# Kernel tuning notes

Measured on AMD Instinct MI355X. Metric: run time of the kernel, lower is better.

## Reference

```python
import math
import jax, jax.numpy as jnp
import numpy as np

N_HEADS = 16

def _alibi_slopes(n_heads: int) -> np.ndarray:
    def pow2_slopes(n):
        start = 2 ** (-2 ** (-(math.log2(n) - 3)))
        return [start * start ** i for i in range(n)]
    if math.log2(n_heads).is_integer():
        slopes = pow2_slopes(n_heads)
    else:
        closest = 2 ** math.floor(math.log2(n_heads))
        slopes = pow2_slopes(closest)
        extra = pow2_slopes(2 * closest)[0::2]
        slopes = slopes + extra[: n_heads - closest]
    return np.asarray(slopes, dtype=np.float32)

def _build_alibi_bias(n_heads: int, T: int) -> jnp.ndarray:
    # (1, H, T, T): lower triangle = -slope*|i-j|, strict upper = -inf (causal)
    slopes = jnp.asarray(_alibi_slopes(n_heads))  # (H,)
    pos = jnp.arange(T)
    dist = pos[None, :] - pos[None, :].T  # (T, T), j - i
    causal = dist < 0  # future positions (j > i means dist>0? note: dist = j - i transposed)
    # match torch: distances = positions[None,:] - positions[:,None] -> dist[i,j] = j - i
    dist = pos[None, :] - pos[:, None]
    causal = dist > 0  # wait: torch masks distances < 0 where distances[i,j] = j - i? No:
    # torch: distances = positions.unsqueeze(0) - positions.unsqueeze(1) -> dist[i,j] = positions[j] - positions[i]? 
    # unsqueeze(0): (1,T) row j; unsqueeze(1): (T,1) row i -> dist[i,j] = pos[j] - pos[i]
    # causal_mask = dist < 0 masks j < i ... but then bias upper triangle kept?
    # Actually torch masks where distances < 0, i.e., j < i (past). That seems inverted,
    # but we must be FAITHFUL: mask fills -inf where pos[j] - pos[i] < 0.
    d = pos[None, :] - pos[:, None]  # d[i,j] = j - i
    mask = d < 0
    bias = -slopes[:, None, None] * jnp.abs(d).astype(jnp.float32)[None, :, :]
    bias = jnp.where(mask[None, :, :], -jnp.inf, bias)
    return bias[None]  # (1, H, T, T)

def setup_inputs() -> dict:
    key = jax.random.key(0)
    k1, k2, k3 = jax.random.split(key, 3)
    B, T, D = 2, 2048, 1024
    x = jax.random.normal(k1, (B, T, D), dtype=jnp.float32)
    W_qkv = jax.random.normal(k2, (D, 3 * D), dtype=jnp.float32) * (1.0 / math.sqrt(D))
    W_out = jax.random.normal(k3, (D, D), dtype=jnp.float32) * (1.0 / math.sqrt(D))
    return {"x": x, "W_qkv": W_qkv, "W_out": W_out}

def reference(x, W_qkv, W_out):
    B, T, D = x.shape
    H = N_HEADS
    hd = D // H
    qkv = x @ W_qkv  # (B, T, 3D)
    q, k, v = jnp.split(qkv, 3, axis=-1)
    q = q.reshape(B, T, H, hd).transpose(0, 2, 1, 3)  # (B,H,T,hd)
    k = k.reshape(B, T, H, hd).transpose(0, 2, 1, 3)
    v = v.reshape(B, T, H, hd).transpose(0, 2, 1, 3)
    scale = 1.0 / math.sqrt(hd)
    attn = jnp.einsum('bhqd,bhkd->bhqk', q, k) * scale  # (B,H,T,T)
    attn = attn + _build_alibi_bias(H, T)
    attn = jax.nn.softmax(attn, axis=-1)
    out = jnp.einsum('bhqk,bhkd->bhqd', attn, v)  # (B,H,T,hd)
    out = out.transpose(0, 2, 1, 3).reshape(B, T, D)
    return out @ W_out
```

## Files before the change

kernel.cpp:

```cpp
#include <hip/hip_runtime.h>

#define DEV __device__ __forceinline__

typedef __attribute__((ext_vector_type(4))) float f32x4;
typedef __attribute__((ext_vector_type(16))) float f32x16;
typedef __attribute__((ext_vector_type(8))) short s16x8;

static constexpr int TB  = 2;
static constexpr int TT  = 2048;
static constexpr int TD  = 1024;
static constexpr int TH  = 16;
static constexpr int THD = 64;
static constexpr int TN3 = 3072;
static constexpr int TM  = TB * TT;

#define WS_FLAG   0u
#define WS_XB     1024u
#define WS_WQKVT  (WS_XB + 8388608u)
#define WS_WOUTT  (WS_WQKVT + 6291456u)
#define WS_QKV    (WS_WOUTT + 2097152u)
#define WS_VT     (WS_QKV + 25165824u)
#define WS_CTX    (WS_VT + 8388608u)

DEV unsigned short f2bf(float f) {
  unsigned int u = __builtin_bit_cast(unsigned int, f);
  u += 0x7FFFu + ((u >> 16) & 1u);
  return (unsigned short)(u >> 16);
}
DEV f32x4 mfma16(s16x8 a, s16x8 b, f32x4 c) {
  return __builtin_amdgcn_mfma_f32_16x16x32_bf16(a, b, c, 0, 0, 0);
}
DEV f32x16 mfma32(s16x8 a, s16x8 b, f32x16 c) {
  return __builtin_amdgcn_mfma_f32_32x32x16_bf16(a, b, c, 0, 0, 0);
}
DEV void gload_lds16(const void* g, void* l) {
  __builtin_amdgcn_global_load_lds(
      (const __attribute__((address_space(1))) void*)g,
      (__attribute__((address_space(3))) void*)l, 16, 0, 0);
}
DEV unsigned int cvtpk(float lo, float hi_) {
  unsigned int r;
  asm("v_cvt_pk_bf16_f32 %0, %1, %2" : "=v"(r) : "v"(lo), "v"(hi_));
  return r;
}
DEV void plswap(unsigned int& a, unsigned int& b) {
  asm("v_permlane32_swap_b32 %0, %1" : "+v"(a), "+v"(b));
}

__global__ __launch_bounds__(256) void detect_kernel(const uint4* __restrict__ probe,
                                                     int* __restrict__ flag) {
  __shared__ int cnt;
  if (threadIdx.x == 0) cnt = 0;
  __syncthreads();
  uint4 v = probe[threadIdx.x];
  int local = 0;
  unsigned int w[4] = {v.x, v.y, v.z, v.w};
#pragma unroll
  for (int k = 0; k < 4; ++k) {
    unsigned int e0 = (w[k] >> 7) & 0xFF;
    unsigned int e1 = (w[k] >> 23) & 0xFF;
    if (e0 >= 135) local++;
    if (e1 >= 135) local++;
  }
  atomicAdd(&cnt, local);
  __syncthreads();
  if (threadIdx.x == 0) flag[0] = (cnt < 100) ? 1 : 0;
}

__global__ __launch_bounds__(256) void prep_kernel(const void* __restrict__ x,
                                                   const void* __restrict__ wqkv,
                                                   const void* __restrict__ wout,
                                                   unsigned short* __restrict__ xb,
                                                   unsigned short* __restrict__ wqkvt,
                                                   unsigned short* __restrict__ woutt,
                                                   const int* __restrict__ flag) {
  __shared__ unsigned short tile[64 * 65];
  const int bid = blockIdx.x;
  const bool bf = (flag[0] != 0);
  if (bid < 1024) {
    const void* W; unsigned short* Wt; int N, k0, n0;
    if (bid < 768) { W = wqkv; Wt = wqkvt; N = TN3; k0 = (bid & 15) * 64; n0 = (bid >> 4) * 64; }
    else { int id = bid - 768; W = wout; Wt = woutt; N = TD; k0 = (id & 15) * 64; n0 = (id >> 4) * 64; }
    for (int e = threadIdx.x; e < 4096; e += 256) {
      int kr = e >> 6, nc = e & 63;
      unsigned short v;
      if (bf) v = ((const unsigned short*)W)[(size_t)(k0 + kr) * N + n0 + nc];
      else    v = f2bf(((const float*)W)[(size_t)(k0 + kr) * N + n0 + nc]);
      tile[kr * 65 + nc] = v;
    }
    __syncthreads();
    for (int e = threadIdx.x; e < 4096; e += 256) {
      int nr = e >> 6, kc = e & 63;
      Wt[(size_t)(n0 + nr) * TD + k0 + kc] = tile[kc * 65 + nr];
    }
  } else {
    int i = (bid - 1024) * 256 + threadIdx.x;
    if (i >= (TM * TD) / 8) return;
    if (bf) {
      ((uint4*)xb)[i] = ((const uint4*)x)[i];
    } else {
      const float* s = (const float*)x + (size_t)i * 8;
      unsigned int w0 = (unsigned int)f2bf(s[0]) | ((unsigned int)f2bf(s[1]) << 16);
      unsigned int w1 = (unsigned int)f2bf(s[2]) | ((unsigned int)f2bf(s[3]) << 16);
      unsigned int w2 = (unsigned int)f2bf(s[4]) | ((unsigned int)f2bf(s[5]) << 16);
      unsigned int w3 = (unsigned int)f2bf(s[6]) | ((unsigned int)f2bf(s[7]) << 16);
      uint4 o; o.x = w0; o.y = w1; o.z = w2; o.w = w3;
      ((uint4*)xb)[i] = o;
    }
  }
}

__global__ __launch_bounds__(512, 2) void gemm_8p_kernel(const unsigned short* __restrict__ A,
                                                         const unsigned short* __restrict__ Bt,
                                                         unsigned short* __restrict__ C,
                                                         unsigned short* __restrict__ vtb,
                                                         int Mn, int Nn, int Kn) {
  __shared__ unsigned short lA[2][256 * 64];
  __shared__ unsigned short lB[2][192 * 64];
  const int tid = threadIdx.x;
  const int lane = tid & 63;
  const int wid = tid >> 6;
  const int wm = wid >> 2, wn = wid & 3;
  const int l15 = lane & 15, lg = lane >> 4;

  const int nby = Nn / 192;
  const int nwg = (Mn >> 8) * nby;
  const int cpx = nwg >> 3;
  const int bid = blockIdx.x;
  const int swz = (bid & 7) * cpx + (bid >> 3);
  const int bm = swz / nby, bn = swz % nby;
  const int row0 = bm << 8, col0 = bn * 192;

  const int srow = tid >> 3;
  const int scol = ((tid & 7) ^ (srow & 7)) * 8;
  const unsigned short* aS = A  + (size_t)(row0 + srow) * Kn + scol;
  const unsigned short* bS = Bt + (size_t)(col0 + srow) * Kn + scol;
  const size_t r64 = (size_t)64 * Kn;

#define STGA(dst, koff) do {                                \
    unsigned short* _d = (dst) + tid * 8;                   \
    const unsigned short* _s = aS + (koff);                 \
    gload_lds16(_s,           _d);                          \
    gload_lds16(_s + r64,     _d + 4096);                   \
    gload_lds16(_s + 2 * r64, _d + 8192);                   \
    gload_lds16(_s + 3 * r64, _d + 12288);                  \
  } while (0)
#define STGB(dst, koff) do {                                \
    unsigned short* _d = (dst) + tid * 8;                   \
    const unsigned short* _s = bS + (koff);                 \
    gload_lds16(_s,           _d);                          \
    gload_lds16(_s + r64,     _d + 4096);                   \
    gload_lds16(_s + 2 * r64, _d + 8192);                   \
  } while (0)

  f32x4 acc[8][3];
#pragma unroll
  for (int m = 0; m < 8; ++m)
#pragma unroll
    for (int n = 0; n < 3; ++n) acc[m][n] = (f32x4){0.f, 0.f, 0.f, 0.f};

  const int sa = l15 & 7;
  const int kc0 = (lg ^ sa) * 8;
  const int kc1 = ((4 + lg) ^ sa) * 8;
  const int aRow = (wm * 128 + l15) * 64;
  const int bRow = (wn * 48 + l15) * 64;

  STGA(&lA[0][0], 0);
  STGB(&lB[0][0], 0);
  asm volatile("s_waitcnt vmcnt(0)" ::: "memory");
  __builtin_amdgcn_s_barrier();

  const int nt = Kn >> 6;
  for (int t = 0; t < nt; ++t) {
    const unsigned short* la = &lA[t & 1][0];
    const unsigned short* lb = &lB[t & 1][0];
    unsigned short* na = &lA[(t + 1) & 1][0];
    unsigned short* nb = &lB[(t + 1) & 1][0];
    const int koff = (t + 1) << 6;
    const bool more = (t + 1 < nt);

    s16x8 af[8], bv[3];

#pragma unroll
    for (int m = 0; m < 8; ++m) af[m] = *(const s16x8*)&la[aRow + m * 1024 + kc0];
#pragma unroll
    for (int n = 0; n < 3; ++n) bv[n] = *(const s16x8*)&lb[bRow + n * 1024 + kc0];
    if (more) STGA(na, koff);
    __builtin_amdgcn_s_barrier();
    asm volatile("s_waitcnt lgkmcnt(0)" ::: "memory");
    __builtin_amdgcn_sched_barrier(0);
    __builtin_amdgcn_s_setprio(1);
#pragma unroll
    for (int m = 0; m < 8; ++m)
#pragma unroll
      for (int n = 0; n < 3; ++n)
        acc[m][n] = mfma16(af[m], bv[n], acc[m][n]);
    __builtin_amdgcn_s_setprio(0);
    __builtin_amdgcn_s_barrier();

#pragma unroll
    for (int m = 0; m < 8; ++m) af[m] = *(const s16x8*)&la[aRow + m * 1024 + kc1];
#pragma unroll
    for (int n = 0; n < 3; ++n) bv[n] = *(const s16x8*)&lb[bRow + n * 1024 + kc1];
    if (more) STGB(nb, koff);
    __builtin_amdgcn_s_barrier();
    asm volatile("s_waitcnt lgkmcnt(0)" ::: "memory");
    __builtin_amdgcn_sched_barrier(0);
    __builtin_amdgcn_s_setprio(1);
#pragma unroll
    for (int m = 0; m < 8; ++m)
#pragma unroll
      for (int n = 0; n < 3; ++n)
        acc[m][n] = mfma16(af[m], bv[n], acc[m][n]);
    __builtin_amdgcn_s_setprio(0);
    asm volatile("s_waitcnt vmcnt(0)" ::: "memory");
    __builtin_amdgcn_s_barrier();
  }
#undef STGA
#undef STGB

  unsigned short* cw = C + (size_t)(row0 + wm * 128 + lg * 4) * Nn + col0 + wn * 48 + l15;
#pragma unroll
  for (int m = 0; m < 8; ++m)
#pragma unroll
    for (int n = 0; n < 3; ++n) {
      const int cbase = col0 + wn * 48 + n * 16;
      if (cbase < 2048) {
#pragma unroll
        for (int j = 0; j < 4; ++j)
          cw[(size_t)(m * 16 + j) * Nn + n * 16] = f2bf(acc[m][n][j]);
      } else {
        int tg = row0 + wm * 128 + lg * 4 + m * 16;
        int bb = tg >> 11, tt = tg & 2047;
        int cc2 = cbase + l15 - 2048;
        int h = cc2 >> 6, d = cc2 & 63;
        unsigned short* dst = vtb + (((size_t)(bb * 16 + h) * 64 + d) << 11) + tt;
        uint2 pk;
        pk.x = cvtpk(acc[m][n][0], acc[m][n][1]);
        pk.y = cvtpk(acc[m][n][2], acc[m][n][3]);
        *(uint2*)dst = pk;
      }
    }
}

__global__ __launch_bounds__(256, 2) void gemm_bt2_kernel(const unsigned short* __restrict__ A,
                                                          const unsigned short* __restrict__ Bt,
                                                          void* __restrict__ Cout,
                                                          int Mn, int Nn, int Kn,
                                                          const int* __restrict__ flag) {
  __shared__ unsigned short lA[3][128 * 64];
  __shared__ unsigned short lB[3][64 * 64];
  const int tid  = threadIdx.x;
  const int lane = tid & 63, wid = tid >> 6;
  const int wr = wid >> 1, wc = wid & 1;
  const int l15 = lane & 15, lg = lane >> 4;
  const int row0 = blockIdx.x * 128, col0 = blockIdx.y * 64;

  f32x4 acc[4][2];
#pragma unroll
  for (int m = 0; m < 4; ++m)
#pragma unroll
    for (int n = 0; n < 2; ++n) acc[m][n] = (f32x4){0.f, 0.f, 0.f, 0.f};

  const int srow = tid >> 3;
  const int scol = ((tid & 7) ^ (srow & 7)) * 8;
  const unsigned short* aS = A  + (size_t)(row0 + srow) * Kn + scol;
  const unsigned short* bS = Bt + (size_t)(col0 + srow) * Kn + scol;
  const size_t r32 = (size_t)32 * Kn;

#define STG2(bi, koff) do {                                                 \
    unsigned short* _da = &lA[bi][0] + tid * 8;                             \
    unsigned short* _db = &lB[bi][0] + tid * 8;                             \
    gload_lds16(aS + (koff),            _da);                               \
    gload_lds16(aS + (koff) + r32,      _da + 2048);                        \
    gload_lds16(aS + (koff) + 2 * r32,  _da + 4096);                        \
    gload_lds16(aS + (koff) + 3 * r32,  _da + 6144);                        \
    gload_lds16(bS + (koff),            _db);                               \
    gload_lds16(bS + (koff) + r32,      _db + 2048);                        \
  } while (0)

  const int sa = l15 & 7;
  const int kc0 = (lg ^ sa) * 8;
  const int kc1 = ((4 + lg) ^ sa) * 8;
  const int aoff = (wr * 64 + l15) * 64;
  const int boff = (wc * 32 + l15) * 64;

  const int nt = Kn >> 6;
  STG2(0, 0);
  STG2(1, 64);
  asm volatile("s_waitcnt vmcnt(6)" ::: "memory");
  __builtin_amdgcn_s_barrier();

  int cur = 0;
  for (int t = 0; t < nt; ++t) {
    const unsigned short* la = &lA[cur][0];
    const unsigned short* lb = &lB[cur][0];
    const bool deep = (t + 2 < nt);

    s16x8 af[4], bfv[2];
#pragma unroll
    for (int m = 0; m < 4; ++m) af[m] = *(const s16x8*)&la[aoff + m * 1024 + kc0];
#pragma unroll
    for (int n = 0; n < 2; ++n) bfv[n] = *(const s16x8*)&lb[boff + n * 1024 + kc0];
    if (deep) { int nbuf = (cur + 2 == 3) ? 0 : ((cur + 2 == 4) ? 1 : cur + 2); STG2(nbuf, (t + 2) << 6); }
    __builtin_amdgcn_s_barrier();
    asm volatile("s_waitcnt lgkmcnt(0)" ::: "memory");
    __builtin_amdgcn_sched_barrier(0);
    __builtin_amdgcn_s_setprio(1);
#pragma unroll
    for (int m = 0; m < 4; ++m)
#pragma unroll
      for (int n = 0; n < 2; ++n)
        acc[m][n] = mfma16(af[m], bfv[n], acc[m][n]);
    __builtin_amdgcn_s_setprio(0);
    __builtin_amdgcn_s_barrier();

#pragma unroll
    for (int m = 0; m < 4; ++m) af[m] = *(const s16x8*)&la[aoff + m * 1024 + kc1];
#pragma unroll
    for (int n = 0; n < 2; ++n) bfv[n] = *(const s16x8*)&lb[boff + n * 1024 + kc1];
    __builtin_amdgcn_s_barrier();
    asm volatile("s_waitcnt lgkmcnt(0)" ::: "memory");
    __builtin_amdgcn_sched_barrier(0);
    __builtin_amdgcn_s_setprio(1);
#pragma unroll
    for (int m = 0; m < 4; ++m)
#pragma unroll
      for (int n = 0; n < 2; ++n)
        acc[m][n] = mfma16(af[m], bfv[n], acc[m][n]);
    __builtin_amdgcn_s_setprio(0);
    if (t + 1 < nt) {
      if (deep) asm volatile("s_waitcnt vmcnt(6)" ::: "memory");
      else      asm volatile("s_waitcnt vmcnt(0)" ::: "memory");
      __builtin_amdgcn_s_barrier();
    }
    cur = (cur == 2) ? 0 : cur + 1;
  }
#undef STG2

  const bool obf = (flag[0] != 0);
#pragma unroll
  for (int m = 0; m < 4; ++m)
#pragma unroll
    for (int n = 0; n < 2; ++n)
#pragma unroll
      for (int j = 0; j < 4; ++j) {
        int r = row0 + wr * 64 + m * 16 + lg * 4 + j;
        int c = col0 + wc * 32 + n * 16 + l15;
        if (obf) ((unsigned short*)Cout)[(size_t)r * Nn + c] = f2bf(acc[m][n][j]);
        else     ((float*)Cout)[(size_t)r * Nn + c] = acc[m][n][j];
      }
}

__global__ __launch_bounds__(256, 4) void attn_kernel(const unsigned short* __restrict__ qkv,
                                                      const unsigned short* __restrict__ vt,
                                                      unsigned short* __restrict__ ctx) {
  __shared__ __align__(16) unsigned char smem[32768];
  unsigned short* kl0 = (unsigned short*)smem;
  unsigned short* vl0 = (unsigned short*)(smem + 16384);
  float* red = (float*)smem;

  const int bid = blockIdx.x;
  const int r_ = bid & 255, q_ = bid >> 8;
  const int s_ = r_ >> 5, g_ = r_ & 31;
  const int bh = (g_ + 8 * q_) & 31;
  const int x32 = (q_ == 0) ? s_ : (q_ == 1) ? 15 - s_ : (q_ == 2) ? 16 + s_ : 31 - s_;
  const int b = bh >> 4, h = bh & 15;

  const int tid = threadIdx.x;
  const int wid = tid >> 6, lane = tid & 63;
  const int wr = wid & 1, wk = wid >> 1;
  const int l31 = lane & 31, hi = lane >> 5;
  const int i_base = x32 * 64 + wr * 32;

  const unsigned short* qb  = qkv + (size_t)b * TT * TN3 + h * THD;
  const unsigned short* kb_ = qkv + (size_t)b * TT * TN3 + TD + h * THD;
  const unsigned short* vb_ = vt + (size_t)bh * THD * TT;

  const float LOG2E = 1.44269504f;
  const float SL2 = exp2f(-0.5f * (float)(h + 1)) * LOG2E;
  const float SC2 = 0.125f * LOG2E;
  const float dbias = -SL2 * 64.0f;

  const int t_rel = (int)((140.0f / SL2 + 63.0f) * (1.0f / 64.0f)) + 1;
  const int t_end = (32 < x32 + t_rel) ? 32 : x32 + t_rel;

  const int srow = tid >> 3;
  const int sx = ((tid & 7) ^ (srow & 7)) * 8;
  const unsigned short* srcK = kb_ + (size_t)(x32 * 64 + srow) * TN3 + sx;
  const unsigned short* srcV = vb_ + (size_t)srow * TT + x32 * 64 + sx;
  const size_t kstep = (size_t)64 * TN3;

#define STAGE(bufi) do {                                   \
    unsigned short* _dk = kl0 + (bufi) * 4096 + tid * 8;   \
    unsigned short* _dv = vl0 + (bufi) * 4096 + tid * 8;   \
    gload_lds16(srcK,            _dk);                     \
    gload_lds16(srcK + 32 * TN3, _dk + 2048);              \
    gload_lds16(srcV,            _dv);                     \
    gload_lds16(srcV + 32 * TT,  _dv + 2048);              \
  } while (0)

  s16x8 qa[4];
  {
    const unsigned short* qr = qb + (size_t)(i_base + l31) * TN3 + hi * 8;
#pragma unroll
    for (int dd = 0; dd < 4; ++dd) qa[dd] = *(const s16x8*)(qr + dd * 16);
  }

  s16x8 ones;
  {
    short ov = (l31 == 0) ? (short)0x3F80 : (short)0;
#pragma unroll
    for (int e = 0; e < 8; ++e) ones[e] = ov;
  }

  float base[16];
#pragma unroll
  for (int r = 0; r < 16; ++r) {
    int cr0 = (r & 3) + 8 * (r >> 2);
    base[r] = -SL2 * (float)(wk * 32 + cr0 + 4 * hi - wr * 32 - l31) - 16.0f;
  }

  f32x16 o0, o1, ol;
#pragma unroll
  for (int r = 0; r < 16; ++r) { o0[r] = 0.f; o1[r] = 0.f; ol[r] = 0.f; }

  const int sw = (l31 & 7) << 4;
  int cc[4];
#pragma unroll
  for (int dd = 0; dd < 4; ++dd) cc[dd] = ((dd * 32 + hi * 16) ^ sw) >> 1;

  int cur = 0;
  STAGE(0); srcK += kstep; srcV += 64;
  asm volatile("s_waitcnt vmcnt(0)" ::: "memory");
  __syncthreads();

  for (int t = x32; t < t_end; ++t) {
    if (t + 1 < t_end) { STAGE(cur ^ 1); srcK += kstep; srcV += 64; }

    const unsigned short* kb = kl0 + cur * 4096;
    const unsigned short* vbl = vl0 + cur * 4096;

    f32x16 sv;
#pragma unroll
    for (int r = 0; r < 16; ++r) sv[r] = 0.f;
    __builtin_amdgcn_s_setprio(1);
#pragma unroll
    for (int dd = 0; dd < 4; ++dd) {
      s16x8 k0 = *(const s16x8*)&kb[(wk * 32 + l31) * 64 + cc[dd]];
      sv = mfma32(k0, qa[dd], sv);
    }
    __builtin_amdgcn_s_setprio(0);

    if (t == x32) {
#pragma unroll
      for (int r = 0; r < 16; ++r) {
        float bb = base[r];
        float v = __builtin_amdgcn_exp2f(fmaf(sv[r], SC2, bb));
        sv[r] = (bb > -15.999f) ? 0.0f : v;
      }
    } else {
#pragma unroll
      for (int r = 0; r < 16; ++r)
        sv[r] = __builtin_amdgcn_exp2f(fmaf(sv[r], SC2, base[r]));
    }
#pragma unroll
    for (int r = 0; r < 16; ++r) base[r] += dbias;

    s16x8 pa[2];
#pragma unroll
    for (int mh = 0; mh < 2; ++mh) {
      unsigned int a0 = cvtpk(sv[8 * mh + 0], sv[8 * mh + 1]);
      unsigned int a1 = cvtpk(sv[8 * mh + 2], sv[8 * mh + 3]);
      unsigned int b0 = cvtpk(sv[8 * mh + 4], sv[8 * mh + 5]);
      unsigned int b1 = cvtpk(sv[8 * mh + 6], sv[8 * mh + 7]);
      plswap(a0, b0); plswap(a1, b1);
      uint4 u; u.x = a0; u.y = a1; u.z = b0; u.w = b1;
      pa[mh] = __builtin_bit_cast(s16x8, u);
    }

    __builtin_amdgcn_s_setprio(1);
#pragma unroll
    for (int ks = 0; ks < 2; ++ks) {
      s16x8 v0 = *(const s16x8*)&vbl[l31 * 64 + cc[wk * 2 + ks]];
      s16x8 v1 = *(const s16x8*)&vbl[(32 + l31) * 64 + cc[wk * 2 + ks]];
      o0 = mfma32(pa[ks], v0, o0);
      o1 = mfma32(pa[ks], v1, o1);
      ol = mfma32(pa[ks], ones, ol);
    }
    __builtin_amdgcn_s_setprio(0);

    asm volatile("s_waitcnt vmcnt(0)" ::: "memory");
    __syncthreads();
    cur ^= 1;
  }
#undef STAGE

  const int rbase = (wr * 64 + lane) * 49;
  if (wk == 1) {
#pragma unroll
    for (int r = 0; r < 16; ++r) red[rbase + r] = o0[r];
#pragma unroll
    for (int r = 0; r < 16; ++r) red[rbase + 16 + r] = o1[r];
#pragma unroll
    for (int r = 0; r < 16; ++r) red[rbase + 32 + r] = ol[r];
  }
  __syncthreads();
  if (wk == 0) {
#pragma unroll
    for (int r = 0; r < 16; ++r) o0[r] += red[rbase + r];
#pragma unroll
    for (int r = 0; r < 16; ++r) o1[r] += red[rbase + 16 + r];
#pragma unroll
    for (int r = 0; r < 16; ++r) ol[r] += red[rbase + 32 + r];

    float rdiv[16];
#pragma unroll
    for (int r = 0; r < 16; ++r) rdiv[r] = 1.0f / __shfl(ol[r], lane & 32);

    unsigned short* cb = ctx + (size_t)(b * TT + i_base) * TD + h * THD + l31;
#pragma unroll
    for (int r = 0; r < 16; ++r) {
      int row = (r & 3) + 8 * (r >> 2) + 4 * hi;
      unsigned int pk = cvtpk(o0[r] * rdiv[r], o1[r] * rdiv[r]);
      cb[(size_t)row * TD] = (unsigned short)pk;
      cb[(size_t)row * TD + 32] = (unsigned short)(pk >> 16);
    }
  }
}

extern "C" void kernel_launch(void* const* d_in, const int* in_sizes, int n_in,
                              void* d_out, int out_size, void* d_ws, size_t ws_size,
                              hipStream_t stream) {
  const void* x    = d_in[0];
  const void* wqkv = d_in[1];
  const void* wout = d_in[2];
  char* ws = (char*)d_ws;
  int* flag             = (int*)(ws + WS_FLAG);
  unsigned short* xb    = (unsigned short*)(ws + WS_XB);
  unsigned short* wqkvt = (unsigned short*)(ws + WS_WQKVT);
  unsigned short* woutt = (unsigned short*)(ws + WS_WOUTT);
  unsigned short* qkvb  = (unsigned short*)(ws + WS_QKV);
  unsigned short* vtb   = (unsigned short*)(ws + WS_VT);
  unsigned short* ctxb  = (unsigned short*)(ws + WS_CTX);

  detect_kernel<<<1, 256, 0, stream>>>((const uint4*)x, flag);
  prep_kernel<<<3072, 256, 0, stream>>>(x, wqkv, wout, xb, wqkvt, woutt, flag);
  gemm_8p_kernel<<<(TM / 256) * (TN3 / 192), 512, 0, stream>>>(xb, wqkvt, qkvb, vtb, TM, TN3, TD);
  attn_kernel<<<1024, 256, 0, stream>>>(qkvb, vtb, ctxb);
  gemm_bt2_kernel<<<dim3(TM / 128, TD / 64), 256, 0, stream>>>(ctxb, woutt, d_out, TM, TD, TD, flag);
}
```

Baseline: 103.1 us.

## Skip bf16 input copy and simplify QKV GEMM k-loop to single-barrier schedule

When the input is already bf16, the prep kernel no longer copies x into the workspace, and the QKV GEMM reads x directly through a flag-selected base pointer. The main k-loop now issues both A and B global-to-LDS prefetches at the start of each iteration. It then loads both k-halves of fragments at once and runs all MFMAs in one block, dropping the intermediate barriers and priority hints. This cuts barrier count and a redundant copy, at the cost of more register pressure and less fine-grained interleaving of loads and MFMAs. The prefetch now writes the other LDS buffer while this iteration reads the current one, so safety relies on the trailing barrier.

```diff
diff --git a/kernel.cpp b/kernel.cpp
--- a/kernel.cpp
+++ b/kernel.cpp
@@ -94,27 +94,26 @@
       Wt[(size_t)(n0 + nr) * TD + k0 + kc] = tile[kc * 65 + nr];
     }
   } else {
+    if (bf) return;
     int i = (bid - 1024) * 256 + threadIdx.x;
     if (i >= (TM * TD) / 8) return;
-    if (bf) {
-      ((uint4*)xb)[i] = ((const uint4*)x)[i];
-    } else {
-      const float* s = (const float*)x + (size_t)i * 8;
-      unsigned int w0 = (unsigned int)f2bf(s[0]) | ((unsigned int)f2bf(s[1]) << 16);
-      unsigned int w1 = (unsigned int)f2bf(s[2]) | ((unsigned int)f2bf(s[3]) << 16);
-      unsigned int w2 = (unsigned int)f2bf(s[4]) | ((unsigned int)f2bf(s[5]) << 16);
-      unsigned int w3 = (unsigned int)f2bf(s[6]) | ((unsigned int)f2bf(s[7]) << 16);
-      uint4 o; o.x = w0; o.y = w1; o.z = w2; o.w = w3;
-      ((uint4*)xb)[i] = o;
-    }
-  }
-}
-
-__global__ __launch_bounds__(512, 2) void gemm_8p_kernel(const unsigned short* __restrict__ A,
+    const float* s = (const float*)x + (size_t)i * 8;
+    unsigned int w0 = (unsigned int)f2bf(s[0]) | ((unsigned int)f2bf(s[1]) << 16);
+    unsigned int w1 = (unsigned int)f2bf(s[2]) | ((unsigned int)f2bf(s[3]) << 16);
+    unsigned int w2 = (unsigned int)f2bf(s[4]) | ((unsigned int)f2bf(s[5]) << 16);
+    unsigned int w3 = (unsigned int)f2bf(s[6]) | ((unsigned int)f2bf(s[7]) << 16);
+    uint4 o; o.x = w0; o.y = w1; o.z = w2; o.w = w3;
+    ((uint4*)xb)[i] = o;
+  }
+}
+
+__global__ __launch_bounds__(512, 2) void gemm_8p_kernel(const unsigned short* __restrict__ Axb,
+                                                         const unsigned short* __restrict__ xraw,
                                                          const unsigned short* __restrict__ Bt,
                                                          unsigned short* __restrict__ C,
                                                          unsigned short* __restrict__ vtb,
-                                                         int Mn, int Nn, int Kn) {
+                                                         int Mn, int Nn, int Kn,
+                                                         const int* __restrict__ flag) {
   __shared__ unsigned short lA[2][256 * 64];
   __shared__ unsigned short lB[2][192 * 64];
   const int tid = threadIdx.x;
@@ -131,9 +130,11 @@
   const int bm = swz / nby, bn = swz % nby;
   const int row0 = bm << 8, col0 = bn * 192;
 
+  const unsigned short* Abase = flag[0] ? xraw : Axb;
+
   const int srow = tid >> 3;
   const int scol = ((tid & 7) ^ (srow & 7)) * 8;
-  const unsigned short* aS = A  + (size_t)(row0 + srow) * Kn + scol;
+  const unsigned short* aS = Abase + (size_t)(row0 + srow) * Kn + scol;
   const unsigned short* bS = Bt + (size_t)(col0 + srow) * Kn + scol;
   const size_t r64 = (size_t)64 * Kn;
 
@@ -179,40 +180,27 @@
     const int koff = (t + 1) << 6;
     const bool more = (t + 1 < nt);
 
-    s16x8 af[8], bv[3];
-
-#pragma unroll
-    for (int m = 0; m < 8; ++m) af[m] = *(const s16x8*)&la[aRow + m * 1024 + kc0];
-#pragma unroll
-    for (int n = 0; n < 3; ++n) bv[n] = *(const s16x8*)&lb[bRow + n * 1024 + kc0];
-    if (more) STGA(na, koff);
-    __builtin_amdgcn_s_barrier();
-    asm volatile("s_waitcnt lgkmcnt(0)" ::: "memory");
-    __builtin_amdgcn_sched_barrier(0);
-    __builtin_amdgcn_s_setprio(1);
+    if (more) { STGA(na, koff); STGB(nb, koff); }
+
+    s16x8 a0[8], a1[8], b0[3], b1[3];
+#pragma unroll
+    for (int m = 0; m < 8; ++m) {
+      a0[m] = *(const s16x8*)&la[aRow + m * 1024 + kc0];
+      a1[m] = *(const s16x8*)&la[aRow + m * 1024 + kc1];
+    }
+#pragma unroll
+    for (int n = 0; n < 3; ++n) {
+      b0[n] = *(const s16x8*)&lb[bRow + n * 1024 + kc0];
+      b1[n] = *(const s16x8*)&lb[bRow + n * 1024 + kc1];
+    }
 #pragma unroll
     for (int m = 0; m < 8; ++m)
 #pragma unroll
-      for (int n = 0; n < 3; ++n)
-        acc[m][n] = mfma16(af[m], bv[n], acc[m][n]);
-    __builtin_amdgcn_s_setprio(0);
-    __builtin_amdgcn_s_barrier();
-
-#pragma unroll
-    for (int m = 0; m < 8; ++m) af[m] = *(const s16x8*)&la[aRow + m * 1024 + kc1];
-#pragma unroll
-    for (int n = 0; n < 3; ++n) bv[n] = *(const s16x8*)&lb[bRow + n * 1024 + kc1];
-    if (more) STGB(nb, koff);
-    __builtin_amdgcn_s_barrier();
-    asm volatile("s_waitcnt lgkmcnt(0)" ::: "memory");
-    __builtin_amdgcn_sched_barrier(0);
-    __builtin_amdgcn_s_setprio(1);
-#pragma unroll
-    for (int m = 0; m < 8; ++m)
-#pragma unroll
-      for (int n = 0; n < 3; ++n)
-        acc[m][n] = mfma16(af[m], bv[n], acc[m][n]);
-    __builtin_amdgcn_s_setprio(0);
+      for (int n = 0; n < 3; ++n) {
+        acc[m][n] = mfma16(a0[m], b0[n], acc[m][n]);
+        acc[m][n] = mfma16(a1[m], b1[n], acc[m][n]);
+      }
+
     asm volatile("s_waitcnt vmcnt(0)" ::: "memory");
     __builtin_amdgcn_s_barrier();
   }
@@ -546,7 +534,7 @@
 
   detect_kernel<<<1, 256, 0, stream>>>((const uint4*)x, flag);
   prep_kernel<<<3072, 256, 0, stream>>>(x, wqkv, wout, xb, wqkvt, woutt, flag);
-  gemm_8p_kernel<<<(TM / 256) * (TN3 / 192), 512, 0, stream>>>(xb, wqkvt, qkvb, vtb, TM, TN3, TD);
+  gemm_8p_kernel<<<(TM / 256) * (TN3 / 192), 512, 0, stream>>>(xb, (const unsigned short*)x, wqkvt, qkvb, vtb, TM, TN3, TD, flag);
   attn_kernel<<<1024, 256, 0, stream>>>(qkvb, vtb, ctxb);
   gemm_bt2_kernel<<<dim3(TM / 128, TD / 64), 256, 0, stream>>>(ctxb, woutt, d_out, TM, TD, TD, flag);
 }
```

Result: no change. 104.7 us (+1.5%).
